# Performance work log

Hardware: AMD Instinct MI355X
Metric: run time of the kernel (lower is better)

## Reference

```python
import jax, jax.numpy as jnp
import numpy as np

LN_EPS = 1e-5
TOP_K = 2


def _layernorm(x):
    # parameter-free LayerNorm over last dim (elementwise_affine=False)
    mu = jnp.mean(x, axis=-1, keepdims=True)
    var = jnp.var(x, axis=-1, keepdims=True)
    return (x - mu) * jax.lax.rsqrt(var + LN_EPS)


def setup_inputs() -> dict:
    key = jax.random.key(0)
    k1, k2 = jax.random.split(key)
    inp = jax.random.normal(k1, (4, 4096, 2048), dtype=jnp.float32)
    emb = jax.random.normal(k2, (64, 2048), dtype=jnp.float32)
    return {"input": inp, "expert_embeddings": emb}


def reference(input, expert_embeddings):
    # standardize both the tokens and the expert embedding table
    x = _layernorm(input)                      # [b, s, d]
    e = _layernorm(expert_embeddings)          # [E, d]
    sim = jnp.einsum("bsd,ed->bse", x, e)      # [b, s, E]
    temp = jnp.sqrt(jnp.asarray(x.shape[-1], x.dtype))  # t=-1 -> sqrt(d)
    weights, module_indices = jax.lax.top_k(sim, TOP_K)  # [b, s, k]
    gates = jax.nn.softmax(weights / temp, axis=-1)
    return (module_indices, gates)
```

## Files before the change

### kernel.cpp

```cpp
#include <hip/hip_runtime.h>
#include <math.h>

#define D 2048
#define NE 64
#define NTOK 16384
#define KSPLIT 4
#define KRANGE (D / KSPLIT)
#define CHUNK 32
#define NCHUNK (KRANGE / CHUNK)
#define TBLK 64
#define XPAD 68
#define LN_EPS 1e-5f

__global__ __launch_bounds__(256) void expert_ln_kernel(
    const float* __restrict__ emb, float* __restrict__ eT) {
  const int e = blockIdx.x;
  const int tid = threadIdx.x;
  const float4* row = (const float4*)(emb + (size_t)e * D);
  float4 v0 = row[tid * 2];
  float4 v1 = row[tid * 2 + 1];
  float s = v0.x + v0.y + v0.z + v0.w + v1.x + v1.y + v1.z + v1.w;
  float q = v0.x * v0.x + v0.y * v0.y + v0.z * v0.z + v0.w * v0.w
          + v1.x * v1.x + v1.y * v1.y + v1.z * v1.z + v1.w * v1.w;
  #pragma unroll
  for (int off = 32; off > 0; off >>= 1) {
    s += __shfl_down(s, off);
    q += __shfl_down(q, off);
  }
  __shared__ float red[8];
  const int wid = tid >> 6;
  const int lane = tid & 63;
  if (lane == 0) { red[wid] = s; red[4 + wid] = q; }
  __syncthreads();
  if (tid == 0) {
    red[0] = red[0] + red[1] + red[2] + red[3];
    red[4] = red[4] + red[5] + red[6] + red[7];
  }
  __syncthreads();
  const float mu = red[0] * (1.0f / D);
  const float var = red[4] * (1.0f / D) - mu * mu;
  const float sc = rsqrtf(var + LN_EPS);
  float vals[8] = {v0.x, v0.y, v0.z, v0.w, v1.x, v1.y, v1.z, v1.w};
  const int k0 = tid * 8;
  #pragma unroll
  for (int j = 0; j < 8; ++j) {
    eT[(size_t)(k0 + j) * NE + e] = (vals[j] - mu) * sc;
  }
}

__global__ __launch_bounds__(256, 4) void router_gemm_kernel(
    const float* __restrict__ x, const float* __restrict__ eT,
    float* __restrict__ dotP, float* __restrict__ sumP,
    float* __restrict__ sumsqP) {
  __shared__ float xT[CHUNK][XPAD];
  __shared__ float eS[CHUNK][NE];
  const int tid = threadIdx.x;
  const int bt = blockIdx.x & 255;
  const int kc = blockIdx.x >> 8;
  const int K0 = kc * KRANGE;
  const int tg = tid & 15;
  const int eg = tid >> 4;

  const int stokA = tid >> 3;
  const int skq = tid & 7;
  const int sekA = tid >> 4;
  const int seq = tid & 15;

  float acc[4][4];
  #pragma unroll
  for (int i = 0; i < 4; ++i)
    #pragma unroll
    for (int j = 0; j < 4; ++j) acc[i][j] = 0.f;
  float sA = 0.f, qA = 0.f, sB = 0.f, qB = 0.f;

  const float* xbase = x + (size_t)bt * TBLK * D + K0;
  const float* ebase = eT + (size_t)K0 * NE;

  float4 px0 = *(const float4*)(xbase + (size_t)stokA * D + skq * 4);
  float4 px1 = *(const float4*)(xbase + (size_t)(stokA + 32) * D + skq * 4);
  float4 pe0 = *(const float4*)(ebase + (size_t)sekA * NE + seq * 4);
  float4 pe1 = *(const float4*)(ebase + (size_t)(sekA + 16) * NE + seq * 4);

  for (int c = 0; c < NCHUNK; ++c) {
    __syncthreads();
    sA += px0.x + px0.y + px0.z + px0.w;
    qA += px0.x * px0.x + px0.y * px0.y + px0.z * px0.z + px0.w * px0.w;
    sB += px1.x + px1.y + px1.z + px1.w;
    qB += px1.x * px1.x + px1.y * px1.y + px1.z * px1.z + px1.w * px1.w;
    xT[skq * 4 + 0][stokA] = px0.x;
    xT[skq * 4 + 1][stokA] = px0.y;
    xT[skq * 4 + 2][stokA] = px0.z;
    xT[skq * 4 + 3][stokA] = px0.w;
    xT[skq * 4 + 0][stokA + 32] = px1.x;
    xT[skq * 4 + 1][stokA + 32] = px1.y;
    xT[skq * 4 + 2][stokA + 32] = px1.z;
    xT[skq * 4 + 3][stokA + 32] = px1.w;
    *(float4*)&eS[sekA][seq * 4] = pe0;
    *(float4*)&eS[sekA + 16][seq * 4] = pe1;
    __syncthreads();
    if (c + 1 < NCHUNK) {
      const int off = (c + 1) * CHUNK;
      px0 = *(const float4*)(xbase + (size_t)stokA * D + off + skq * 4);
      px1 = *(const float4*)(xbase + (size_t)(stokA + 32) * D + off + skq * 4);
      pe0 = *(const float4*)(ebase + (size_t)(off + sekA) * NE + seq * 4);
      pe1 = *(const float4*)(ebase + (size_t)(off + sekA + 16) * NE + seq * 4);
    }
    #pragma unroll 8
    for (int kk = 0; kk < CHUNK; ++kk) {
      const float4 a = *(const float4*)&xT[kk][tg * 4];
      const float4 b = *(const float4*)&eS[kk][eg * 4];
      const float ar[4] = {a.x, a.y, a.z, a.w};
      const float br[4] = {b.x, b.y, b.z, b.w};
      #pragma unroll
      for (int i = 0; i < 4; ++i)
        #pragma unroll
        for (int j = 0; j < 4; ++j)
          acc[i][j] = fmaf(ar[i], br[j], acc[i][j]);
    }
  }

  {
    float* dp = dotP + ((size_t)kc * NTOK + (size_t)bt * TBLK + tg * 4) * NE + eg * 4;
    #pragma unroll
    for (int i = 0; i < 4; ++i) {
      *(float4*)(dp + (size_t)i * NE) =
          make_float4(acc[i][0], acc[i][1], acc[i][2], acc[i][3]);
    }
  }

  __syncthreads();
  float* r1 = &xT[0][0];
  float* r2 = &xT[0][0] + 512;
  r1[skq * 64 + stokA] = sA;
  r1[skq * 64 + 32 + stokA] = sB;
  r2[skq * 64 + stokA] = qA;
  r2[skq * 64 + 32 + stokA] = qB;
  __syncthreads();
  if (tid < TBLK) {
    float s = 0.f, q = 0.f;
    #pragma unroll
    for (int j = 0; j < 8; ++j) {
      s += r1[j * 64 + tid];
      q += r2[j * 64 + tid];
    }
    const int gt = bt * TBLK + tid;
    sumP[kc * NTOK + gt] = s;
    sumsqP[kc * NTOK + gt] = q;
  }
}

__global__ __launch_bounds__(256) void finalize_kernel(
    const float* __restrict__ dotP, const float* __restrict__ sumP,
    const float* __restrict__ sumsqP, float* __restrict__ out) {
  const int tid = threadIdx.x;
  const int t = blockIdx.x * 32 + (tid >> 3);
  const int l8 = tid & 7;

  float s1 = 0.f, s2 = 0.f;
  #pragma unroll
  for (int kc = 0; kc < KSPLIT; ++kc) {
    s1 += sumP[kc * NTOK + t];
    s2 += sumsqP[kc * NTOK + t];
  }
  const float mu = s1 * (1.0f / D);
  const float var = s2 * (1.0f / D) - mu * mu;
  const float sc = rsqrtf(var + LN_EPS);

  float d[8] = {0.f, 0.f, 0.f, 0.f, 0.f, 0.f, 0.f, 0.f};
  #pragma unroll
  for (int kc = 0; kc < KSPLIT; ++kc) {
    const float* dp = dotP + ((size_t)kc * NTOK + t) * NE + l8 * 8;
    float4 a = *(const float4*)dp;
    float4 b = *(const float4*)(dp + 4);
    d[0] += a.x; d[1] += a.y; d[2] += a.z; d[3] += a.w;
    d[4] += b.x; d[5] += b.y; d[6] += b.z; d[7] += b.w;
  }

  float w1 = -INFINITY, w2 = -INFINITY;
  int i1 = 0, i2 = 0;
  #pragma unroll
  for (int j = 0; j < 8; ++j) {
    const float v = d[j] * sc;
    const int e = l8 * 8 + j;
    if (v > w1) { w2 = w1; i2 = i1; w1 = v; i1 = e; }
    else if (v > w2) { w2 = v; i2 = e; }
  }
  #pragma unroll
  for (int off = 1; off < 8; off <<= 1) {
    const float ow1 = __shfl_xor(w1, off);
    const float ow2 = __shfl_xor(w2, off);
    const int oi1 = __shfl_xor(i1, off);
    const int oi2 = __shfl_xor(i2, off);
    if (ow1 > w1 || (ow1 == w1 && oi1 < i1)) {
      float nw2; int ni2;
      if (w1 > ow2 || (w1 == ow2 && i1 < oi2)) { nw2 = w1; ni2 = i1; }
      else { nw2 = ow2; ni2 = oi2; }
      w1 = ow1; i1 = oi1; w2 = nw2; i2 = ni2;
    } else {
      if (ow1 > w2 || (ow1 == w2 && oi1 < i2)) { w2 = ow1; i2 = oi1; }
    }
  }

  if (l8 == 0) {
    const float invT = 0.02209708691207961f;
    const float e1 = expf((w2 - w1) * invT);
    const float g1 = 1.0f / (1.0f + e1);
    const float g2 = e1 * g1;
    out[t * 2 + 0] = (float)i1;
    out[t * 2 + 1] = (float)i2;
    out[2 * NTOK + t * 2 + 0] = g1;
    out[2 * NTOK + t * 2 + 1] = g2;
  }
}

extern "C" void kernel_launch(void* const* d_in, const int* in_sizes, int n_in,
                              void* d_out, int out_size, void* d_ws, size_t ws_size,
                              hipStream_t stream) {
  const float* x = (const float*)d_in[0];
  const float* emb = (const float*)d_in[1];
  float* ws = (float*)d_ws;
  float* eT = ws;
  float* dotP = ws + 131072;
  float* sumP = dotP + (size_t)KSPLIT * NTOK * NE;
  float* sumsqP = sumP + (size_t)KSPLIT * NTOK;
  float* out = (float*)d_out;

  expert_ln_kernel<<<NE, 256, 0, stream>>>(emb, eT);
  router_gemm_kernel<<<KSPLIT * (NTOK / TBLK), 256, 0, stream>>>(
      x, eT, dotP, sumP, sumsqP);
  finalize_kernel<<<NTOK / 32, 256, 0, stream>>>(dotP, sumP, sumsqP, out);
}
```

Measured before the change: 218.5 us.

## Fuse router GEMM with LN stats and top-2 epilogue, drop split-K partials

Removes the split-K decomposition and the separate finalize kernel. Each 512-thread block now covers the full D range for 64 tokens, computes the row statistics, and does the top-2 selection and softmax gating in-block. This eliminates the round trip of partial dot products and sums through global memory, plus one kernel launch. In exchange the grid drops from 1024 to 256 blocks, each with a longer serial K loop and a smaller per-thread register tile (2x4), which could lower parallelism and arithmetic intensity on a many-CU GPU.

```diff
diff --git a/kernel.cpp b/kernel.cpp
--- a/kernel.cpp
+++ b/kernel.cpp
@@ -4,12 +4,11 @@
 #define D 2048
 #define NE 64
 #define NTOK 16384
-#define KSPLIT 4
-#define KRANGE (D / KSPLIT)
-#define CHUNK 32
-#define NCHUNK (KRANGE / CHUNK)
 #define TBLK 64
-#define XPAD 68
+#define THREADS 512
+#define CHUNK 64
+#define NCHUNK (D / CHUNK)
+#define XPAD 66
 #define LN_EPS 1e-5f
 
 __global__ __launch_bounds__(256) void expert_ln_kernel(
@@ -48,38 +47,34 @@
   }
 }
 
-__global__ __launch_bounds__(256, 4) void router_gemm_kernel(
+__global__ __launch_bounds__(THREADS) void router_fused_kernel(
     const float* __restrict__ x, const float* __restrict__ eT,
-    float* __restrict__ dotP, float* __restrict__ sumP,
-    float* __restrict__ sumsqP) {
+    float* __restrict__ out) {
   __shared__ float xT[CHUNK][XPAD];
   __shared__ float eS[CHUNK][NE];
+  __shared__ float scs[TBLK];
   const int tid = threadIdx.x;
-  const int bt = blockIdx.x & 255;
-  const int kc = blockIdx.x >> 8;
-  const int K0 = kc * KRANGE;
-  const int tg = tid & 15;
-  const int eg = tid >> 4;
+  const int bt = blockIdx.x;
+  const int tg = tid >> 4;
+  const int eg = tid & 15;
 
-  const int stokA = tid >> 3;
-  const int skq = tid & 7;
-  const int sekA = tid >> 4;
-  const int seq = tid & 15;
+  const int stok = tid >> 4;
+  const int skq = tid & 15;
 
-  float acc[4][4];
+  float acc[2][4];
   #pragma unroll
-  for (int i = 0; i < 4; ++i)
+  for (int i = 0; i < 2; ++i)
     #pragma unroll
     for (int j = 0; j < 4; ++j) acc[i][j] = 0.f;
   float sA = 0.f, qA = 0.f, sB = 0.f, qB = 0.f;
 
-  const float* xbase = x + (size_t)bt * TBLK * D + K0;
-  const float* ebase = eT + (size_t)K0 * NE;
+  const float* xbase = x + (size_t)bt * TBLK * D;
+  const float* ebase = eT;
 
-  float4 px0 = *(const float4*)(xbase + (size_t)stokA * D + skq * 4);
-  float4 px1 = *(const float4*)(xbase + (size_t)(stokA + 32) * D + skq * 4);
-  float4 pe0 = *(const float4*)(ebase + (size_t)sekA * NE + seq * 4);
-  float4 pe1 = *(const float4*)(ebase + (size_t)(sekA + 16) * NE + seq * 4);
+  float4 px0 = *(const float4*)(xbase + (size_t)stok * D + skq * 4);
+  float4 px1 = *(const float4*)(xbase + (size_t)(stok + 32) * D + skq * 4);
+  float4 pe0 = *(const float4*)(ebase + (size_t)stok * NE + skq * 4);
+  float4 pe1 = *(const float4*)(ebase + (size_t)(stok + 32) * NE + skq * 4);
 
   for (int c = 0; c < NCHUNK; ++c) {
     __syncthreads();
@@ -87,129 +82,107 @@
     qA += px0.x * px0.x + px0.y * px0.y + px0.z * px0.z + px0.w * px0.w;
     sB += px1.x + px1.y + px1.z + px1.w;
     qB += px1.x * px1.x + px1.y * px1.y + px1.z * px1.z + px1.w * px1.w;
-    xT[skq * 4 + 0][stokA] = px0.x;
-    xT[skq * 4 + 1][stokA] = px0.y;
-    xT[skq * 4 + 2][stokA] = px0.z;
-    xT[skq * 4 + 3][stokA] = px0.w;
-    xT[skq * 4 + 0][stokA + 32] = px1.x;
-    xT[skq * 4 + 1][stokA + 32] = px1.y;
-    xT[skq * 4 + 2][stokA + 32] = px1.z;
-    xT[skq * 4 + 3][stokA + 32] = px1.w;
-    *(float4*)&eS[sekA][seq * 4] = pe0;
-    *(float4*)&eS[sekA + 16][seq * 4] = pe1;
-    __syncthreads();
+    xT[skq * 4 + 0][stok] = px0.x;
+    xT[skq * 4 + 1][stok] = px0.y;
+    xT[skq * 4 + 2][stok] = px0.z;
+    xT[skq * 4 + 3][stok] = px0.w;
+    xT[skq * 4 + 0][stok + 32] = px1.x;
+    xT[skq * 4 + 1][stok + 32] = px1.y;
+    xT[skq * 4 + 2][stok + 32] = px1.z;
+    xT[skq * 4 + 3][stok + 32] = px1.w;
+    *(float4*)&eS[stok][skq * 4] = pe0;
+    *(float4*)&eS[stok + 32][skq * 4] = pe1;
     if (c + 1 < NCHUNK) {
       const int off = (c + 1) * CHUNK;
-      px0 = *(const float4*)(xbase + (size_t)stokA * D + off + skq * 4);
-      px1 = *(const float4*)(xbase + (size_t)(stokA + 32) * D + off + skq * 4);
-      pe0 = *(const float4*)(ebase + (size_t)(off + sekA) * NE + seq * 4);
-      pe1 = *(const float4*)(ebase + (size_t)(off + sekA + 16) * NE + seq * 4);
+      px0 = *(const float4*)(xbase + (size_t)stok * D + off + skq * 4);
+      px1 = *(const float4*)(xbase + (size_t)(stok + 32) * D + off + skq * 4);
+      pe0 = *(const float4*)(ebase + (size_t)(off + stok) * NE + skq * 4);
+      pe1 = *(const float4*)(ebase + (size_t)(off + stok + 32) * NE + skq * 4);
     }
-    #pragma unroll 8
+    __syncthreads();
+    #pragma unroll 16
     for (int kk = 0; kk < CHUNK; ++kk) {
-      const float4 a = *(const float4*)&xT[kk][tg * 4];
+      const float2 a = *(const float2*)&xT[kk][tg * 2];
       const float4 b = *(const float4*)&eS[kk][eg * 4];
-      const float ar[4] = {a.x, a.y, a.z, a.w};
-      const float br[4] = {b.x, b.y, b.z, b.w};
-      #pragma unroll
-      for (int i = 0; i < 4; ++i)
-        #pragma unroll
-        for (int j = 0; j < 4; ++j)
-          acc[i][j] = fmaf(ar[i], br[j], acc[i][j]);
-    }
-  }
-
-  {
-    float* dp = dotP + ((size_t)kc * NTOK + (size_t)bt * TBLK + tg * 4) * NE + eg * 4;
-    #pragma unroll
-    for (int i = 0; i < 4; ++i) {
-      *(float4*)(dp + (size_t)i * NE) =
-          make_float4(acc[i][0], acc[i][1], acc[i][2], acc[i][3]);
+      acc[0][0] = fmaf(a.x, b.x, acc[0][0]);
+      acc[0][1] = fmaf(a.x, b.y, acc[0][1]);
+      acc[0][2] = fmaf(a.x, b.z, acc[0][2]);
+      acc[0][3] = fmaf(a.x, b.w, acc[0][3]);
+      acc[1][0] = fmaf(a.y, b.x, acc[1][0]);
+      acc[1][1] = fmaf(a.y, b.y, acc[1][1]);
+      acc[1][2] = fmaf(a.y, b.z, acc[1][2]);
+      acc[1][3] = fmaf(a.y, b.w, acc[1][3]);
     }
   }
 
   __syncthreads();
   float* r1 = &xT[0][0];
-  float* r2 = &xT[0][0] + 512;
-  r1[skq * 64 + stokA] = sA;
-  r1[skq * 64 + 32 + stokA] = sB;
-  r2[skq * 64 + stokA] = qA;
-  r2[skq * 64 + 32 + stokA] = qB;
+  float* r2 = &eS[0][0];
+  r1[skq * 64 + stok] = sA;
+  r1[skq * 64 + stok + 32] = sB;
+  r2[skq * 64 + stok] = qA;
+  r2[skq * 64 + stok + 32] = qB;
   __syncthreads();
   if (tid < TBLK) {
     float s = 0.f, q = 0.f;
     #pragma unroll
-    for (int j = 0; j < 8; ++j) {
+    for (int j = 0; j < 16; ++j) {
       s += r1[j * 64 + tid];
       q += r2[j * 64 + tid];
     }
-    const int gt = bt * TBLK + tid;
-    sumP[kc * NTOK + gt] = s;
-    sumsqP[kc * NTOK + gt] = q;
+    const float mu = s * (1.0f / D);
+    const float var = q * (1.0f / D) - mu * mu;
+    scs[tid] = rsqrtf(var + LN_EPS);
   }
-}
+  __syncthreads();
 
-__global__ __launch_bounds__(256) void finalize_kernel(
-    const float* __restrict__ dotP, const float* __restrict__ sumP,
-    const float* __restrict__ sumsqP, float* __restrict__ out) {
-  const int tid = threadIdx.x;
-  const int t = blockIdx.x * 32 + (tid >> 3);
-  const int l8 = tid & 7;
+  const float sc0 = scs[tg * 2];
+  const float sc1 = scs[tg * 2 + 1];
 
-  float s1 = 0.f, s2 = 0.f;
+  float w1[2] = {-INFINITY, -INFINITY}, w2[2] = {-INFINITY, -INFINITY};
+  int i1[2] = {0, 0}, i2[2] = {0, 0};
   #pragma unroll
-  for (int kc = 0; kc < KSPLIT; ++kc) {
-    s1 += sumP[kc * NTOK + t];
-    s2 += sumsqP[kc * NTOK + t];
-  }
-  const float mu = s1 * (1.0f / D);
-  const float var = s2 * (1.0f / D) - mu * mu;
-  const float sc = rsqrtf(var + LN_EPS);
-
-  float d[8] = {0.f, 0.f, 0.f, 0.f, 0.f, 0.f, 0.f, 0.f};
-  #pragma unroll
-  for (int kc = 0; kc < KSPLIT; ++kc) {
-    const float* dp = dotP + ((size_t)kc * NTOK + t) * NE + l8 * 8;
-    float4 a = *(const float4*)dp;
-    float4 b = *(const float4*)(dp + 4);
-    d[0] += a.x; d[1] += a.y; d[2] += a.z; d[3] += a.w;
-    d[4] += b.x; d[5] += b.y; d[6] += b.z; d[7] += b.w;
-  }
-
-  float w1 = -INFINITY, w2 = -INFINITY;
-  int i1 = 0, i2 = 0;
-  #pragma unroll
-  for (int j = 0; j < 8; ++j) {
-    const float v = d[j] * sc;
-    const int e = l8 * 8 + j;
-    if (v > w1) { w2 = w1; i2 = i1; w1 = v; i1 = e; }
-    else if (v > w2) { w2 = v; i2 = e; }
+  for (int j = 0; j < 4; ++j) {
+    const int e = eg * 4 + j;
+    const float v0 = acc[0][j] * sc0;
+    const float v1 = acc[1][j] * sc1;
+    if (v0 > w1[0]) { w2[0] = w1[0]; i2[0] = i1[0]; w1[0] = v0; i1[0] = e; }
+    else if (v0 > w2[0]) { w2[0] = v0; i2[0] = e; }
+    if (v1 > w1[1]) { w2[1] = w1[1]; i2[1] = i1[1]; w1[1] = v1; i1[1] = e; }
+    else if (v1 > w2[1]) { w2[1] = v1; i2[1] = e; }
   }
   #pragma unroll
-  for (int off = 1; off < 8; off <<= 1) {
-    const float ow1 = __shfl_xor(w1, off);
-    const float ow2 = __shfl_xor(w2, off);
-    const int oi1 = __shfl_xor(i1, off);
-    const int oi2 = __shfl_xor(i2, off);
-    if (ow1 > w1 || (ow1 == w1 && oi1 < i1)) {
-      float nw2; int ni2;
-      if (w1 > ow2 || (w1 == ow2 && i1 < oi2)) { nw2 = w1; ni2 = i1; }
-      else { nw2 = ow2; ni2 = oi2; }
-      w1 = ow1; i1 = oi1; w2 = nw2; i2 = ni2;
-    } else {
-      if (ow1 > w2 || (ow1 == w2 && oi1 < i2)) { w2 = ow1; i2 = oi1; }
+  for (int off = 1; off < 16; off <<= 1) {
+    #pragma unroll
+    for (int i = 0; i < 2; ++i) {
+      const float ow1 = __shfl_xor(w1[i], off);
+      const float ow2 = __shfl_xor(w2[i], off);
+      const int oi1 = __shfl_xor(i1[i], off);
+      const int oi2 = __shfl_xor(i2[i], off);
+      if (ow1 > w1[i] || (ow1 == w1[i] && oi1 < i1[i])) {
+        float nw2; int ni2;
+        if (w1[i] > ow2 || (w1[i] == ow2 && i1[i] < oi2)) { nw2 = w1[i]; ni2 = i1[i]; }
+        else { nw2 = ow2; ni2 = oi2; }
+        w1[i] = ow1; i1[i] = oi1; w2[i] = nw2; i2[i] = ni2;
+      } else {
+        if (ow1 > w2[i] || (ow1 == w2[i] && oi1 < i2[i])) { w2[i] = ow1; i2[i] = oi1; }
+      }
     }
   }
 
-  if (l8 == 0) {
+  if (eg == 0) {
     const float invT = 0.02209708691207961f;
-    const float e1 = expf((w2 - w1) * invT);
-    const float g1 = 1.0f / (1.0f + e1);
-    const float g2 = e1 * g1;
-    out[t * 2 + 0] = (float)i1;
-    out[t * 2 + 1] = (float)i2;
-    out[2 * NTOK + t * 2 + 0] = g1;
-    out[2 * NTOK + t * 2 + 1] = g2;
+    #pragma unroll
+    for (int i = 0; i < 2; ++i) {
+      const int t = bt * TBLK + tg * 2 + i;
+      const float e1 = expf((w2[i] - w1[i]) * invT);
+      const float g1 = 1.0f / (1.0f + e1);
+      const float g2 = e1 * g1;
+      out[t * 2 + 0] = (float)i1[i];
+      out[t * 2 + 1] = (float)i2[i];
+      out[2 * NTOK + t * 2 + 0] = g1;
+      out[2 * NTOK + t * 2 + 1] = g2;
+    }
   }
 }
 
@@ -218,15 +191,9 @@
                               hipStream_t stream) {
   const float* x = (const float*)d_in[0];
   const float* emb = (const float*)d_in[1];
-  float* ws = (float*)d_ws;
-  float* eT = ws;
-  float* dotP = ws + 131072;
-  float* sumP = dotP + (size_t)KSPLIT * NTOK * NE;
-  float* sumsqP = sumP + (size_t)KSPLIT * NTOK;
+  float* eT = (float*)d_ws;
   float* out = (float*)d_out;
 
   expert_ln_kernel<<<NE, 256, 0, stream>>>(emb, eT);
-  router_gemm_kernel<<<KSPLIT * (NTOK / TBLK), 256, 0, stream>>>(
-      x, eT, dotP, sumP, sumsqP);
-  finalize_kernel<<<NTOK / 32, 256, 0, stream>>>(dotP, sumP, sumsqP, out);
+  router_fused_kernel<<<NTOK / TBLK, THREADS, 0, stream>>>(x, eT, out);
 }
```

Result: slower. 246.8 us (+13.0%).
